# Optimization experiments

Measured on AMD Instinct MI355X. Metric: run time of the kernel, lower is better.

## Reference

```python
import jax, jax.numpy as jnp
import numpy as np

N_NODES = 50000
N_EDGES = 800000
D = 128
N_GRAPHS = 64
N_CLASSES = 10


def setup_inputs() -> dict:
    key = jax.random.key(0)
    ks = jax.random.split(key, 10)
    x = jax.random.normal(ks[0], (N_NODES, D), dtype=jnp.float32)
    edge_index = jax.random.randint(ks[1], (2, N_EDGES), 0, N_NODES, dtype=jnp.int64)
    batch = jnp.sort(jax.random.randint(ks[2], (N_NODES,), 0, N_GRAPHS, dtype=jnp.int64))
    s = 1.0 / np.sqrt(D)
    W1a = jax.random.uniform(ks[3], (D, D), jnp.float32, -s, s)
    W1b = jax.random.uniform(ks[4], (D, D), jnp.float32, -s, s)
    W2a = jax.random.uniform(ks[5], (D, D), jnp.float32, -s, s)
    W2b = jax.random.uniform(ks[6], (D, D), jnp.float32, -s, s)
    Wfc = jax.random.uniform(ks[7], (D, N_CLASSES), jnp.float32, -s, s)
    return {
        "x": x, "edge_index": edge_index, "batch": batch,
        "W1a": W1a, "b1a": jnp.zeros((D,), jnp.float32),
        "W1b": W1b, "b1b": jnp.zeros((D,), jnp.float32),
        "W2a": W2a, "b2a": jnp.zeros((D,), jnp.float32),
        "W2b": W2b, "b2b": jnp.zeros((D,), jnp.float32),
        "Wfc": Wfc, "bfc": jnp.zeros((N_CLASSES,), jnp.float32),
    }


def _gin_conv(x, src, dst, Wa, ba, Wb, bb):
    # sum aggregation of neighbor messages x[src] into dst (eps = 0)
    agg = jax.ops.segment_sum(x[src], dst, num_segments=N_NODES)
    h = x + agg  # (1 + eps) * x + sum_{j->i} x_j
    h = jax.nn.relu(h @ Wa + ba)
    h = jax.nn.relu(h @ Wb + bb)
    return h


def reference(x, edge_index, batch, W1a, b1a, W1b, b1b, W2a, b2a, W2b, b2b, Wfc, bfc):
    src, dst = edge_index[0], edge_index[1]
    h = _gin_conv(x, src, dst, W1a, b1a, W1b, b1b)
    h = _gin_conv(h, src, dst, W2a, b2a, W2b, b2b)
    # global mean pool over graphs
    sums = jax.ops.segment_sum(h, batch, num_segments=N_GRAPHS)
    counts = jax.ops.segment_sum(jnp.ones((h.shape[0], 1), h.dtype), batch, num_segments=N_GRAPHS)
    pooled = sums / jnp.maximum(counts, 1.0)
    logits = pooled @ Wfc + bfc
    return jax.nn.sigmoid(logits)
```

## Files before the change

kernel.cpp:

```cpp
#include <hip/hip_runtime.h>

#define NN 50000
#define NE 800000
#define DF 128
#define NG 64
#define NC 10
#define NBK 98
#define PART_CHUNK 4096
#define PART_GRID 196
#define ACAP 12288
#define FINE_CAP 12288
#define RT 136
#define CAST_GRID 6250
#define PREP_GRID (CAST_GRID + 32)

typedef short bf16x8 __attribute__((ext_vector_type(8)));
typedef float f32x4  __attribute__((ext_vector_type(4)));

__device__ __forceinline__ void atomAddF(float* p, float v) {
  __hip_atomic_fetch_add(p, v, __ATOMIC_RELAXED, __HIP_MEMORY_SCOPE_AGENT);
}
__device__ __forceinline__ float b2f(unsigned short u) {
  union { unsigned int i; float f; } v; v.i = (unsigned int)u << 16; return v.f;
}
__device__ __forceinline__ unsigned int f2b(float f) {
  unsigned int i = __float_as_uint(f);
  return (i + 0x7fffu + ((i >> 16) & 1u)) >> 16;
}

__global__ __launch_bounds__(256) void k_prep_part(const float* __restrict__ x,
                                                   unsigned short* __restrict__ xb,
                                                   const float* __restrict__ W0,
                                                   const float* __restrict__ W1,
                                                   const float* __restrict__ W2,
                                                   const float* __restrict__ W3,
                                                   unsigned short* __restrict__ Wt,
                                                   const int* __restrict__ src,
                                                   const int* __restrict__ dst,
                                                   int* __restrict__ cnt_b,
                                                   unsigned int* __restrict__ arena)
{
  __shared__ unsigned int stage[PART_CHUNK];
  __shared__ int lhist[128], lcnt[128], lcur[128], gbase[128];
  const int tid = threadIdx.x;
  const int b   = blockIdx.x;

  if (b < CAST_GRID) {
    const int i = b * 256 + tid;
    const float4 v = reinterpret_cast<const float4*>(x)[i];
    uint2 o;
    o.x = f2b(v.x) | (f2b(v.y) << 16);
    o.y = f2b(v.z) | (f2b(v.w) << 16);
    reinterpret_cast<uint2*>(xb)[i] = o;
    return;
  }
  if (b < PREP_GRID) {
    const int o = (b - CAST_GRID) * 256 + tid;
    const int mat = o >> 11;
    const float* W = (mat == 0) ? W0 : (mat == 1) ? W1 : (mat == 2) ? W2 : W3;
    const int rem = o & 2047;
    const int kb = rem >> 7, n = rem & 127;
    unsigned int u[8];
#pragma unroll
    for (int j = 0; j < 8; ++j) u[j] = f2b(W[(size_t)(kb * 8 + j) * DF + n]);
    uint4 p;
    p.x = u[0] | (u[1] << 16);
    p.y = u[2] | (u[3] << 16);
    p.z = u[4] | (u[5] << 16);
    p.w = u[6] | (u[7] << 16);
    *reinterpret_cast<uint4*>(Wt + (size_t)mat * DF * DF + (size_t)rem * 8) = p;
    return;
  }

  const int vb = b - PREP_GRID;
  const int e0 = vb * PART_CHUNK;
  const int nE = min(PART_CHUNK, NE - e0);

  for (int i = tid; i < 128; i += 256) lhist[i] = 0;
  __syncthreads();
  unsigned int pk[16]; int bk[16];
#pragma unroll
  for (int i = 0; i < 16; ++i) {
    const int e = e0 + i * 256 + tid;
    if (e < NE) {
      const int d = dst[e], s = src[e];
      const int bb = d >> 9;
      bk[i] = bb;
      pk[i] = ((unsigned int)bb << 25) | ((unsigned int)(d & 511) << 16) | (unsigned int)s;
      atomicAdd(&lhist[bb], 1);
    } else bk[i] = -1;
  }
  __syncthreads();
  for (int i = tid; i < 128; i += 256) lcnt[i] = lhist[i];
  __syncthreads();
  for (int off = 1; off < 128; off <<= 1) {
    int v = 0;
    if (tid < 128 && tid >= off) v = lhist[tid - off];
    __syncthreads();
    if (tid < 128) lhist[tid] += v;
    __syncthreads();
  }
  if (tid < 128) lcur[tid] = lhist[tid] - lcnt[tid];
  __syncthreads();
#pragma unroll
  for (int i = 0; i < 16; ++i)
    if (bk[i] >= 0) {
      const int pos = atomicAdd(&lcur[bk[i]], 1);
      stage[pos] = pk[i];
    }
  __syncthreads();
  if (tid < NBK) {
    const int c = lcnt[tid];
    if (c > 0) gbase[tid] = atomicAdd(&cnt_b[tid], c);
  }
  __syncthreads();
  for (int idx = tid; idx < nE; idx += 256) {
    const unsigned int p = stage[idx];
    const int bb = (int)(p >> 25);
    const int loff = lhist[bb] - lcnt[bb];
    arena[(size_t)bb * ACAP + gbase[bb] + (idx - loff)] = p;
  }
}

__global__ __launch_bounds__(256) void k_fine(const unsigned int* __restrict__ arena,
                                              const int* __restrict__ cnt_b,
                                              int* __restrict__ rs,
                                              unsigned short* __restrict__ es)
{
  __shared__ unsigned short les[FINE_CAP];
  __shared__ int bins[4096];
  __shared__ int partials[256];
  __shared__ int basebuf[128];
  const int tid = threadIdx.x;
  const int b   = blockIdx.x;

  if (b == 0 && tid == 0) rs[NN] = NE;

  if (tid < 128) basebuf[tid] = (tid < NBK) ? cnt_b[tid] : 0;
  __syncthreads();
  for (int off = 1; off < 128; off <<= 1) {
    int u = 0;
    if (tid < 128 && tid >= off) u = basebuf[tid - off];
    __syncthreads();
    if (tid < 128) basebuf[tid] += u;
    __syncthreads();
  }
  const int wbase = (b == 0) ? 0 : basebuf[b - 1];
  const int cnt   = cnt_b[b];
  const int nbase = b << 9;
  const int nwin  = min(512, NN - nbase);
  const unsigned int* ap = arena + (size_t)b * ACAP;

  for (int i = tid; i < 4096; i += 256) bins[i] = 0;
  __syncthreads();
  for (int idx = tid; idx < cnt; idx += 256) {
    const unsigned int p = ap[idx];
    const int key = (int)(((p >> 16) & 511) << 3) | (int)((p & 0xffffu) >> 13);
    atomicAdd(&bins[key], 1);
  }
  __syncthreads();
  const int b16 = tid * 16;
  int sum = 0;
#pragma unroll
  for (int k = 0; k < 16; ++k) sum += bins[b16 + k];
  partials[tid] = sum;
  __syncthreads();
  for (int off = 1; off < 256; off <<= 1) {
    int u = (tid >= off) ? partials[tid - off] : 0;
    __syncthreads();
    partials[tid] += u;
    __syncthreads();
  }
  int run = partials[tid] - sum;
#pragma unroll
  for (int k = 0; k < 16; ++k) {
    const int v = bins[b16 + k];
    bins[b16 + k] = run;
    run += v;
  }
  __syncthreads();
  for (int i = tid; i < nwin; i += 256) rs[nbase + i] = wbase + bins[i << 3];
  __syncthreads();
  if (cnt <= FINE_CAP) {
    for (int idx = tid; idx < cnt; idx += 256) {
      const unsigned int p = ap[idx];
      const int key = (int)(((p >> 16) & 511) << 3) | (int)((p & 0xffffu) >> 13);
      const int pos = atomicAdd(&bins[key], 1);
      les[pos] = (unsigned short)(p & 0xffffu);
    }
    __syncthreads();
    for (int i = tid; i < cnt; i += 256) es[wbase + i] = les[i];
  } else {
    for (int idx = tid; idx < cnt; idx += 256) {
      const unsigned int p = ap[idx];
      const int key = (int)(((p >> 16) & 511) << 3) | (int)((p & 0xffffu) >> 13);
      const int pos = atomicAdd(&bins[key], 1);
      es[wbase + pos] = (unsigned short)(p & 0xffffu);
    }
  }
}

__global__ __launch_bounds__(256) void k_gather(const unsigned short* __restrict__ feat,
                                                unsigned short* __restrict__ outp,
                                                const int* __restrict__ rs,
                                                const unsigned short* __restrict__ es)
{
  const int wid  = (blockIdx.x * 256 + threadIdx.x) >> 6;
  const int lane = threadIdx.x & 63;
  if (wid >= NN) return;
  const int beg = rs[wid];
  const int end = rs[wid + 1];
  const int off = lane * 2;

  const unsigned int self = *reinterpret_cast<const unsigned int*>(feat + (size_t)wid * DF + off);
  float ax = b2f(self & 0xffff), ay = b2f(self >> 16);
  int j = beg;
  while (j < end && (j & 3)) {
    const unsigned int u = *reinterpret_cast<const unsigned int*>(feat + (size_t)es[j] * DF + off);
    ax += b2f(u & 0xffff); ay += b2f(u >> 16);
    ++j;
  }
  for (; j + 3 < end; j += 4) {
    const uint2 e4 = *reinterpret_cast<const uint2*>(es + j);
    const int s0 = (int)(e4.x & 0xffffu), s1 = (int)(e4.x >> 16);
    const int s2 = (int)(e4.y & 0xffffu), s3 = (int)(e4.y >> 16);
    const unsigned int u0 = *reinterpret_cast<const unsigned int*>(feat + (size_t)s0 * DF + off);
    const unsigned int u1 = *reinterpret_cast<const unsigned int*>(feat + (size_t)s1 * DF + off);
    const unsigned int u2 = *reinterpret_cast<const unsigned int*>(feat + (size_t)s2 * DF + off);
    const unsigned int u3 = *reinterpret_cast<const unsigned int*>(feat + (size_t)s3 * DF + off);
    ax += b2f(u0 & 0xffff) + b2f(u1 & 0xffff) + b2f(u2 & 0xffff) + b2f(u3 & 0xffff);
    ay += b2f(u0 >> 16)    + b2f(u1 >> 16)    + b2f(u2 >> 16)    + b2f(u3 >> 16);
  }
  for (; j < end; ++j) {
    const unsigned int u = *reinterpret_cast<const unsigned int*>(feat + (size_t)es[j] * DF + off);
    ax += b2f(u & 0xffff); ay += b2f(u >> 16);
  }
  const unsigned int o = f2b(ax) | (f2b(ay) << 16);
  *reinterpret_cast<unsigned int*>(outp + (size_t)wid * DF + off) = o;
}

__global__ __launch_bounds__(256, 4) void k_gemm2(const unsigned short* __restrict__ Ab,
                                                  const unsigned short* __restrict__ Wta,
                                                  const float* __restrict__ ba,
                                                  const unsigned short* __restrict__ Wtb,
                                                  const float* __restrict__ bb,
                                                  unsigned short* __restrict__ outb, int M)
{
  __shared__ unsigned short hL[4][16 * RT];
  const int tid  = threadIdx.x;
  const int lane = tid & 63;
  const int w    = tid >> 6;
  const int col  = lane & 15;
  const int kq   = lane >> 4;

  const int m   = blockIdx.x * 64 + w * 16 + col;
  const int mld = (m < M) ? m : (M - 1);

  bf16x8 bc[4];
#pragma unroll
  for (int s = 0; s < 4; ++s)
    bc[s] = *reinterpret_cast<const bf16x8*>(Ab + (size_t)mld * DF + s * 32 + kq * 8);

  f32x4 acc[8];
#pragma unroll
  for (int nf = 0; nf < 8; ++nf) acc[nf] = (f32x4){0.f, 0.f, 0.f, 0.f};
#pragma unroll
  for (int s = 0; s < 4; ++s) {
#pragma unroll
    for (int nf = 0; nf < 8; ++nf) {
      const bf16x8 wa = *reinterpret_cast<const bf16x8*>(
          Wta + ((size_t)(s * 4 + kq) * 128 + nf * 16 + col) * 8);
      acc[nf] = __builtin_amdgcn_mfma_f32_16x16x32_bf16(wa, bc[s], acc[nf], 0, 0, 0);
    }
  }

  unsigned short* hw = &hL[w][0];
#pragma unroll
  for (int nf = 0; nf < 8; ++nf) {
    const float4 bva = *reinterpret_cast<const float4*>(ba + nf * 16 + kq * 4);
    uint2 pk;
    pk.x = f2b(fmaxf(acc[nf][0] + bva.x, 0.f)) | (f2b(fmaxf(acc[nf][1] + bva.y, 0.f)) << 16);
    pk.y = f2b(fmaxf(acc[nf][2] + bva.z, 0.f)) | (f2b(fmaxf(acc[nf][3] + bva.w, 0.f)) << 16);
    *reinterpret_cast<uint2*>(&hw[col * RT + nf * 16 + kq * 4]) = pk;
  }
  asm volatile("s_waitcnt lgkmcnt(0)" ::: "memory");
  __builtin_amdgcn_sched_barrier(0);

  f32x4 acc2[8];
#pragma unroll
  for (int nf = 0; nf < 8; ++nf) acc2[nf] = (f32x4){0.f, 0.f, 0.f, 0.f};
#pragma unroll
  for (int s = 0; s < 4; ++s) {
    const bf16x8 hb = *reinterpret_cast<const bf16x8*>(&hw[col * RT + s * 32 + kq * 8]);
#pragma unroll
    for (int nf = 0; nf < 8; ++nf) {
      const bf16x8 wb = *reinterpret_cast<const bf16x8*>(
          Wtb + ((size_t)(s * 4 + kq) * 128 + nf * 16 + col) * 8);
      acc2[nf] = __builtin_amdgcn_mfma_f32_16x16x32_bf16(wb, hb, acc2[nf], 0, 0, 0);
    }
  }
  if (m < M) {
#pragma unroll
    for (int nf = 0; nf < 8; ++nf) {
      const float4 bvb = *reinterpret_cast<const float4*>(bb + nf * 16 + kq * 4);
      ushort4 p;
      p.x = (unsigned short)f2b(fmaxf(acc2[nf][0] + bvb.x, 0.f));
      p.y = (unsigned short)f2b(fmaxf(acc2[nf][1] + bvb.y, 0.f));
      p.z = (unsigned short)f2b(fmaxf(acc2[nf][2] + bvb.z, 0.f));
      p.w = (unsigned short)f2b(fmaxf(acc2[nf][3] + bvb.w, 0.f));
      *reinterpret_cast<ushort4*>(outb + (size_t)m * DF + nf * 16 + kq * 4) = p;
    }
  }
}

__global__ __launch_bounds__(256) void k_pool(const unsigned short* __restrict__ h,
                                              const int* __restrict__ batch,
                                              float* __restrict__ sums,
                                              int* __restrict__ cnts)
{
  const int wv   = (blockIdx.x * 256 + threadIdx.x) >> 6;
  const int lane = threadIdx.x & 63;
  const int n0 = wv * 32;
  if (n0 >= NN) return;
  const int n1 = min(n0 + 32, NN);
  const int off = lane * 2;

  const int gfirst = batch[n0];
  const int glast  = batch[n1 - 1];
  float ax = 0.f, ay = 0.f;

  if (gfirst == glast) {
#pragma unroll 4
    for (int i = n0; i < n1; ++i) {
      const unsigned int u = *reinterpret_cast<const unsigned int*>(h + (size_t)i * DF + off);
      ax += b2f(u & 0xffff); ay += b2f(u >> 16);
    }
    atomAddF(&sums[gfirst * DF + off],     ax);
    atomAddF(&sums[gfirst * DF + off + 1], ay);
    if (lane == 0) atomicAdd(&cnts[gfirst], n1 - n0);
  } else {
    int g = gfirst, cnt = 0;
    for (int i = n0; i < n1; ++i) {
      const int gi = batch[i];
      if (gi != g) {
        atomAddF(&sums[g * DF + off],     ax);
        atomAddF(&sums[g * DF + off + 1], ay);
        if (lane == 0) atomicAdd(&cnts[g], cnt);
        ax = 0.f; ay = 0.f; cnt = 0; g = gi;
      }
      const unsigned int u = *reinterpret_cast<const unsigned int*>(h + (size_t)i * DF + off);
      ax += b2f(u & 0xffff); ay += b2f(u >> 16);
      ++cnt;
    }
    atomAddF(&sums[g * DF + off],     ax);
    atomAddF(&sums[g * DF + off + 1], ay);
    if (lane == 0) atomicAdd(&cnts[g], cnt);
  }
}

__global__ __launch_bounds__(256) void k_head(const float* __restrict__ sums,
                                              const int* __restrict__ cnts,
                                              const float* __restrict__ Wfc,
                                              const float* __restrict__ bfc,
                                              float* __restrict__ out)
{
  for (int o = threadIdx.x; o < NG * NC; o += 256) {
    const int g = o / NC, c = o % NC;
    const float inv = 1.f / fmaxf((float)cnts[g], 1.f);
    float z = bfc[c];
    for (int k = 0; k < DF; ++k)
      z = fmaf(sums[g * DF + k] * inv, Wfc[k * NC + c], z);
    out[o] = 1.f / (1.f + expf(-z));
  }
}

extern "C" void kernel_launch(void* const* d_in, const int* in_sizes, int n_in,
                              void* d_out, int out_size, void* d_ws, size_t ws_size,
                              hipStream_t stream)
{
  const float* x   = (const float*)d_in[0];
  const int*   ei  = (const int*)d_in[1];
  const int* batch = (const int*)d_in[2];
  const float* W1a = (const float*)d_in[3];
  const float* b1a = (const float*)d_in[4];
  const float* W1b = (const float*)d_in[5];
  const float* b1b = (const float*)d_in[6];
  const float* W2a = (const float*)d_in[7];
  const float* b2a = (const float*)d_in[8];
  const float* W2b = (const float*)d_in[9];
  const float* b2b = (const float*)d_in[10];
  const float* Wfc = (const float*)d_in[11];
  const float* bfc = (const float*)d_in[12];
  float* out = (float*)d_out;

  const int* src = ei;
  const int* dst = ei + NE;

  unsigned short* xb = (unsigned short*)d_ws;
  unsigned short* A  = xb + (size_t)NN * DF;
  unsigned short* H  = A + (size_t)NN * DF;
  unsigned short* Wt = H + (size_t)NN * DF;
  float* sums  = (float*)(Wt + (size_t)4 * DF * DF);
  int*   cnts  = (int*)(sums + NG * DF);
  int*   cnt_b = cnts + 64;
  int*   rs    = cnt_b + 128;
  unsigned short* es = (unsigned short*)(rs + (NN + 4));
  unsigned int* arena = (unsigned int*)(es + NE);

  unsigned short* Wt1a = Wt;
  unsigned short* Wt1b = Wt + DF * DF;
  unsigned short* Wt2a = Wt + 2 * DF * DF;
  unsigned short* Wt2b = Wt + 3 * DF * DF;

  const int gemm_grid   = (NN + 63) / 64;
  const int gather_grid = (NN * 64 + 255) / 256;
  const int pool_grid   = ((NN + 31) / 32 + 3) / 4;

  hipMemsetAsync(sums, 0, (size_t)(NG * DF + 64 + 128) * sizeof(float), stream);
  k_prep_part<<<PREP_GRID + PART_GRID, 256, 0, stream>>>(
      x, xb, W1a, W1b, W2a, W2b, Wt, src, dst, cnt_b, arena);
  k_fine<<<NBK, 256, 0, stream>>>(arena, cnt_b, rs, es);

  k_gather<<<gather_grid, 256, 0, stream>>>(xb, A, rs, es);
  k_gemm2<<<gemm_grid, 256, 0, stream>>>(A, Wt1a, b1a, Wt1b, b1b, A, NN);

  k_gather<<<gather_grid, 256, 0, stream>>>(A, H, rs, es);
  k_gemm2<<<gemm_grid, 256, 0, stream>>>(H, Wt2a, b2a, Wt2b, b2b, H, NN);

  k_pool<<<pool_grid, 256, 0, stream>>>(H, batch, sums, cnts);
  k_head<<<1, 256, 0, stream>>>(sums, cnts, Wfc, bfc, out);
}
```

Before: 196.0 us.

## Split gather wave into half-waves over edges and fuse pooling with head

The neighbor gather now lets each half of a wave handle alternate edges. Each lane loads 8 bytes (four bf16 values) per row, and the two halves are combined with a cross-half shuffle, so more independent row loads are in flight per wave. The pooling kernel absorbs the classifier head through a last-block-done atomic counter, which removes one kernel launch. An explicit LDS waitcnt and scheduling barrier are also dropped from the fused GEMM, leaving ordering to the compiler. The costs are an extra shuffle reduction, idle half-waves on odd-degree tails, and a serialized head computed by a single block.

```diff
diff --git a/kernel.cpp b/kernel.cpp
--- a/kernel.cpp
+++ b/kernel.cpp
@@ -13,6 +13,7 @@
 #define RT 136
 #define CAST_GRID 6250
 #define PREP_GRID (CAST_GRID + 32)
+#define POOL_GRID 391
 
 typedef short bf16x8 __attribute__((ext_vector_type(8)));
 typedef float f32x4  __attribute__((ext_vector_type(4)));
@@ -208,35 +209,58 @@
   const int wid  = (blockIdx.x * 256 + threadIdx.x) >> 6;
   const int lane = threadIdx.x & 63;
   if (wid >= NN) return;
+  const int half = lane >> 5;
+  const int l32  = lane & 31;
+  const int off  = l32 * 4;
   const int beg = rs[wid];
   const int end = rs[wid + 1];
-  const int off = lane * 2;
-
-  const unsigned int self = *reinterpret_cast<const unsigned int*>(feat + (size_t)wid * DF + off);
-  float ax = b2f(self & 0xffff), ay = b2f(self >> 16);
+
+  float a0 = 0.f, a1 = 0.f, a2 = 0.f, a3 = 0.f;
+  if (!half) {
+    const uint2 u = *reinterpret_cast<const uint2*>(feat + (size_t)wid * DF + off);
+    a0 = b2f(u.x & 0xffff); a1 = b2f(u.x >> 16);
+    a2 = b2f(u.y & 0xffff); a3 = b2f(u.y >> 16);
+  }
+
   int j = beg;
-  while (j < end && (j & 3)) {
-    const unsigned int u = *reinterpret_cast<const unsigned int*>(feat + (size_t)es[j] * DF + off);
-    ax += b2f(u & 0xffff); ay += b2f(u >> 16);
-    ++j;
-  }
-  for (; j + 3 < end; j += 4) {
-    const uint2 e4 = *reinterpret_cast<const uint2*>(es + j);
-    const int s0 = (int)(e4.x & 0xffffu), s1 = (int)(e4.x >> 16);
-    const int s2 = (int)(e4.y & 0xffffu), s3 = (int)(e4.y >> 16);
-    const unsigned int u0 = *reinterpret_cast<const unsigned int*>(feat + (size_t)s0 * DF + off);
-    const unsigned int u1 = *reinterpret_cast<const unsigned int*>(feat + (size_t)s1 * DF + off);
-    const unsigned int u2 = *reinterpret_cast<const unsigned int*>(feat + (size_t)s2 * DF + off);
-    const unsigned int u3 = *reinterpret_cast<const unsigned int*>(feat + (size_t)s3 * DF + off);
-    ax += b2f(u0 & 0xffff) + b2f(u1 & 0xffff) + b2f(u2 & 0xffff) + b2f(u3 & 0xffff);
-    ay += b2f(u0 >> 16)    + b2f(u1 >> 16)    + b2f(u2 >> 16)    + b2f(u3 >> 16);
-  }
-  for (; j < end; ++j) {
-    const unsigned int u = *reinterpret_cast<const unsigned int*>(feat + (size_t)es[j] * DF + off);
-    ax += b2f(u & 0xffff); ay += b2f(u >> 16);
-  }
-  const unsigned int o = f2b(ax) | (f2b(ay) << 16);
-  *reinterpret_cast<unsigned int*>(outp + (size_t)wid * DF + off) = o;
+  for (; j + 7 < end; j += 8) {
+    const int i0 = es[j + half];
+    const int i1 = es[j + 2 + half];
+    const int i2 = es[j + 4 + half];
+    const int i3 = es[j + 6 + half];
+    const uint2 u0 = *reinterpret_cast<const uint2*>(feat + (size_t)i0 * DF + off);
+    const uint2 u1 = *reinterpret_cast<const uint2*>(feat + (size_t)i1 * DF + off);
+    const uint2 u2 = *reinterpret_cast<const uint2*>(feat + (size_t)i2 * DF + off);
+    const uint2 u3 = *reinterpret_cast<const uint2*>(feat + (size_t)i3 * DF + off);
+    a0 += b2f(u0.x & 0xffff) + b2f(u1.x & 0xffff) + b2f(u2.x & 0xffff) + b2f(u3.x & 0xffff);
+    a1 += b2f(u0.x >> 16)    + b2f(u1.x >> 16)    + b2f(u2.x >> 16)    + b2f(u3.x >> 16);
+    a2 += b2f(u0.y & 0xffff) + b2f(u1.y & 0xffff) + b2f(u2.y & 0xffff) + b2f(u3.y & 0xffff);
+    a3 += b2f(u0.y >> 16)    + b2f(u1.y >> 16)    + b2f(u2.y >> 16)    + b2f(u3.y >> 16);
+  }
+  for (; j + 1 < end; j += 2) {
+    const int i = es[j + half];
+    const uint2 u = *reinterpret_cast<const uint2*>(feat + (size_t)i * DF + off);
+    a0 += b2f(u.x & 0xffff); a1 += b2f(u.x >> 16);
+    a2 += b2f(u.y & 0xffff); a3 += b2f(u.y >> 16);
+  }
+  if (j < end && !half) {
+    const int i = es[j];
+    const uint2 u = *reinterpret_cast<const uint2*>(feat + (size_t)i * DF + off);
+    a0 += b2f(u.x & 0xffff); a1 += b2f(u.x >> 16);
+    a2 += b2f(u.y & 0xffff); a3 += b2f(u.y >> 16);
+  }
+
+  a0 += __shfl_xor(a0, 32);
+  a1 += __shfl_xor(a1, 32);
+  a2 += __shfl_xor(a2, 32);
+  a3 += __shfl_xor(a3, 32);
+
+  if (!half) {
+    uint2 o;
+    o.x = f2b(a0) | (f2b(a1) << 16);
+    o.y = f2b(a2) | (f2b(a3) << 16);
+    *reinterpret_cast<uint2*>(outp + (size_t)wid * DF + off) = o;
+  }
 }
 
 __global__ __launch_bounds__(256, 4) void k_gemm2(const unsigned short* __restrict__ Ab,
@@ -283,8 +307,6 @@
     pk.y = f2b(fmaxf(acc[nf][2] + bva.z, 0.f)) | (f2b(fmaxf(acc[nf][3] + bva.w, 0.f)) << 16);
     *reinterpret_cast<uint2*>(&hw[col * RT + nf * 16 + kq * 4]) = pk;
   }
-  asm volatile("s_waitcnt lgkmcnt(0)" ::: "memory");
-  __builtin_amdgcn_sched_barrier(0);
 
   f32x4 acc2[8];
 #pragma unroll
@@ -316,61 +338,73 @@
 __global__ __launch_bounds__(256) void k_pool(const unsigned short* __restrict__ h,
                                               const int* __restrict__ batch,
                                               float* __restrict__ sums,
-                                              int* __restrict__ cnts)
-{
-  const int wv   = (blockIdx.x * 256 + threadIdx.x) >> 6;
-  const int lane = threadIdx.x & 63;
-  const int n0 = wv * 32;
-  if (n0 >= NN) return;
-  const int n1 = min(n0 + 32, NN);
-  const int off = lane * 2;
-
-  const int gfirst = batch[n0];
-  const int glast  = batch[n1 - 1];
-  float ax = 0.f, ay = 0.f;
-
-  if (gfirst == glast) {
-#pragma unroll 4
-    for (int i = n0; i < n1; ++i) {
-      const unsigned int u = *reinterpret_cast<const unsigned int*>(h + (size_t)i * DF + off);
-      ax += b2f(u & 0xffff); ay += b2f(u >> 16);
-    }
-    atomAddF(&sums[gfirst * DF + off],     ax);
-    atomAddF(&sums[gfirst * DF + off + 1], ay);
-    if (lane == 0) atomicAdd(&cnts[gfirst], n1 - n0);
-  } else {
-    int g = gfirst, cnt = 0;
-    for (int i = n0; i < n1; ++i) {
-      const int gi = batch[i];
-      if (gi != g) {
-        atomAddF(&sums[g * DF + off],     ax);
-        atomAddF(&sums[g * DF + off + 1], ay);
-        if (lane == 0) atomicAdd(&cnts[g], cnt);
-        ax = 0.f; ay = 0.f; cnt = 0; g = gi;
-      }
-      const unsigned int u = *reinterpret_cast<const unsigned int*>(h + (size_t)i * DF + off);
-      ax += b2f(u & 0xffff); ay += b2f(u >> 16);
-      ++cnt;
-    }
-    atomAddF(&sums[g * DF + off],     ax);
-    atomAddF(&sums[g * DF + off + 1], ay);
-    if (lane == 0) atomicAdd(&cnts[g], cnt);
-  }
-}
-
-__global__ __launch_bounds__(256) void k_head(const float* __restrict__ sums,
-                                              const int* __restrict__ cnts,
+                                              int* __restrict__ cnts,
+                                              int* __restrict__ done,
                                               const float* __restrict__ Wfc,
                                               const float* __restrict__ bfc,
                                               float* __restrict__ out)
 {
-  for (int o = threadIdx.x; o < NG * NC; o += 256) {
-    const int g = o / NC, c = o % NC;
-    const float inv = 1.f / fmaxf((float)cnts[g], 1.f);
-    float z = bfc[c];
-    for (int k = 0; k < DF; ++k)
-      z = fmaf(sums[g * DF + k] * inv, Wfc[k * NC + c], z);
-    out[o] = 1.f / (1.f + expf(-z));
+  const int tid  = threadIdx.x;
+  const int wv   = (blockIdx.x * 256 + tid) >> 6;
+  const int lane = tid & 63;
+  const int n0 = wv * 32;
+
+  if (n0 < NN) {
+    const int n1 = min(n0 + 32, NN);
+    const int off = lane * 2;
+    const int gfirst = batch[n0];
+    const int glast  = batch[n1 - 1];
+    float ax = 0.f, ay = 0.f;
+
+    if (gfirst == glast) {
+#pragma unroll 4
+      for (int i = n0; i < n1; ++i) {
+        const unsigned int u = *reinterpret_cast<const unsigned int*>(h + (size_t)i * DF + off);
+        ax += b2f(u & 0xffff); ay += b2f(u >> 16);
+      }
+      atomAddF(&sums[gfirst * DF + off],     ax);
+      atomAddF(&sums[gfirst * DF + off + 1], ay);
+      if (lane == 0) atomicAdd(&cnts[gfirst], n1 - n0);
+    } else {
+      int g = gfirst, cnt = 0;
+      for (int i = n0; i < n1; ++i) {
+        const int gi = batch[i];
+        if (gi != g) {
+          atomAddF(&sums[g * DF + off],     ax);
+          atomAddF(&sums[g * DF + off + 1], ay);
+          if (lane == 0) atomicAdd(&cnts[g], cnt);
+          ax = 0.f; ay = 0.f; cnt = 0; g = gi;
+        }
+        const unsigned int u = *reinterpret_cast<const unsigned int*>(h + (size_t)i * DF + off);
+        ax += b2f(u & 0xffff); ay += b2f(u >> 16);
+        ++cnt;
+      }
+      atomAddF(&sums[g * DF + off],     ax);
+      atomAddF(&sums[g * DF + off + 1], ay);
+      if (lane == 0) atomicAdd(&cnts[g], cnt);
+    }
+  }
+
+  __shared__ int amLast;
+  __syncthreads();
+  if (tid == 0) {
+    __threadfence();
+    amLast = (atomicAdd(done, 1) == POOL_GRID - 1) ? 1 : 0;
+  }
+  __syncthreads();
+  if (amLast) {
+    __threadfence();
+    for (int o = tid; o < NG * NC; o += 256) {
+      const int g = o / NC, c = o % NC;
+      const int cg = __hip_atomic_load(&cnts[g], __ATOMIC_RELAXED, __HIP_MEMORY_SCOPE_AGENT);
+      const float inv = 1.f / fmaxf((float)cg, 1.f);
+      float z = bfc[c];
+      for (int k = 0; k < DF; ++k) {
+        const float sv = __hip_atomic_load(&sums[g * DF + k], __ATOMIC_RELAXED, __HIP_MEMORY_SCOPE_AGENT);
+        z = fmaf(sv * inv, Wfc[k * NC + c], z);
+      }
+      out[o] = 1.f / (1.f + expf(-z));
+    }
   }
 }
 
@@ -403,7 +437,8 @@
   float* sums  = (float*)(Wt + (size_t)4 * DF * DF);
   int*   cnts  = (int*)(sums + NG * DF);
   int*   cnt_b = cnts + 64;
-  int*   rs    = cnt_b + 128;
+  int*   done  = cnt_b + 128;
+  int*   rs    = done + 4;
   unsigned short* es = (unsigned short*)(rs + (NN + 4));
   unsigned int* arena = (unsigned int*)(es + NE);
 
@@ -414,9 +449,8 @@
 
   const int gemm_grid   = (NN + 63) / 64;
   const int gather_grid = (NN * 64 + 255) / 256;
-  const int pool_grid   = ((NN + 31) / 32 + 3) / 4;
-
-  hipMemsetAsync(sums, 0, (size_t)(NG * DF + 64 + 128) * sizeof(float), stream);
+
+  hipMemsetAsync(sums, 0, (size_t)(NG * DF + 64 + 128 + 4) * sizeof(float), stream);
   k_prep_part<<<PREP_GRID + PART_GRID, 256, 0, stream>>>(
       x, xb, W1a, W1b, W2a, W2b, Wt, src, dst, cnt_b, arena);
   k_fine<<<NBK, 256, 0, stream>>>(arena, cnt_b, rs, es);
@@ -427,6 +461,5 @@
   k_gather<<<gather_grid, 256, 0, stream>>>(A, H, rs, es);
   k_gemm2<<<gemm_grid, 256, 0, stream>>>(H, Wt2a, b2a, Wt2b, b2b, H, NN);
 
-  k_pool<<<pool_grid, 256, 0, stream>>>(H, batch, sums, cnts);
-  k_head<<<1, 256, 0, stream>>>(sums, cnts, Wfc, bfc, out);
-}
+  k_pool<<<POOL_GRID, 256, 0, stream>>>(H, batch, sums, cnts, done, Wfc, bfc, out);
+}
```

Result: slower. 203.9 us (+4.1%).
